# Kernel optimization log

Hardware: AMD Instinct MI355X
Metric: run time of the kernel (lower is better)

## Reference

```python
import jax, jax.numpy as jnp
import numpy as np

N, K, M = 4096, 128, 512  # conformers, dihedrals, atoms


def setup_inputs() -> dict:
    key = jax.random.key(0)
    k1, k2 = jax.random.split(key)
    inp = jax.random.normal(k1, (N, K), dtype=jnp.float32)          # target dihedral deltas (rad)
    pos0 = jax.random.normal(k2, (N, M, 3), dtype=jnp.float32)      # initial conformer coordinates
    base = jnp.arange(K, dtype=jnp.int32)
    # chain molecule: dihedral k defined by atoms (k, k+1, k+2, k+3)
    angles = jnp.stack([base, base + 1, base + 2, base + 3], axis=1)  # (K, 4)
    # rdkit toBeMovedIdxList on a chain for bond (k+1, k+2): atoms k+3 .. M-1 move
    move_mask = jnp.arange(M)[None, :] > (base + 2)[:, None]          # (K, M) bool
    return {"input": inp, "pos0": pos0, "angles": angles, "move_mask": move_mask}


def _rot_matrix(theta, axis):
    # rdkit Transform3D::SetRotation: R = (1-cos)*aa^T + [[c,-sZ,sY],[sZ,c,-sX],[-sY,sX,c]]
    cosT = jnp.cos(theta)
    sinT = jnp.sin(theta)
    t = 1.0 - cosT
    outer = t[:, None, None] * axis[:, :, None] * axis[:, None, :]   # (N,3,3)
    X, Y, Z = axis[:, 0], axis[:, 1], axis[:, 2]
    mat1 = jnp.stack(
        [cosT, -sinT * Z, sinT * Y,
         sinT * Z, cosT, -sinT * X,
         -sinT * Y, sinT * X, cosT], axis=1
    ).reshape(-1, 3, 3)
    return outer + mat1


def _step(pos, x):
    ang, mask, theta = x                       # (4,), (M,), (N,)
    p = jnp.take(pos, ang, axis=1)             # (N,4,3) gather of i,j,k,l atoms
    rIJ = p[:, 1] - p[:, 0]
    rJK = p[:, 2] - p[:, 1]
    rKL = p[:, 3] - p[:, 2]
    nIJK = jnp.cross(rIJ, rJK)
    nJKL = jnp.cross(rJK, rKL)
    m = jnp.cross(nIJK, rJK)
    nrm = lambda v: jnp.linalg.norm(v, axis=-1)
    sin_arg = jnp.sum(m * nJKL, axis=-1) / (nrm(nJKL) * nrm(m))
    cos_arg = jnp.sum(nIJK * nJKL, axis=-1) / (nrm(nIJK) * nrm(nJKL))
    values = theta + jnp.arctan2(sin_arg, cos_arg)   # rotation angle per conformer
    begin = p[:, 1]                                   # rotation axis origin (atom j)
    d = p[:, 2] - p[:, 1]
    # torch.nn.functional.normalize with eps=1e-12
    axis = d / jnp.maximum(jnp.linalg.norm(d, axis=-1, keepdims=True), 1e-12)
    R = _rot_matrix(values, axis)                     # (N,3,3)
    rotated = jnp.einsum('nij,nmj->nmi', R, pos - begin[:, None, :]) + begin[:, None, :]
    pos = jnp.where(mask[None, :, None], rotated, pos)
    return pos, None


def reference(input, pos0, angles, move_mask):
    xs = (angles, move_mask, input.T)                 # scan over K dihedrals (sequential recurrence)
    pos, _ = jax.lax.scan(_step, pos0, xs)
    return pos
```

## Files before the change

### kernel.cpp

```cpp
#include <hip/hip_runtime.h>


#define NK 128
#define NM 512
#define NMOL 4096
#define TPB 256
#define WPB 4
#define MPW 2

struct Aff { float qw, qx, qy, qz, tx, ty, tz; };

__device__ __forceinline__ void qrot(float qw, float qx, float qy, float qz,
                                     float vx, float vy, float vz,
                                     float& ox, float& oy, float& oz) {
    const float ux = qy*vz - qz*vy + qw*vx;
    const float uy = qz*vx - qx*vz + qw*vy;
    const float uz = qx*vy - qy*vx + qw*vz;
    ox = vx + 2.f*(qy*uz - qz*uy);
    oy = vy + 2.f*(qz*ux - qx*uz);
    oz = vz + 2.f*(qx*uy - qy*ux);
}

__device__ __forceinline__ Aff aff_compose(const Aff& Q, const Aff& P) {
    Aff r;
    r.qw = Q.qw*P.qw - Q.qx*P.qx - Q.qy*P.qy - Q.qz*P.qz;
    r.qx = Q.qw*P.qx + Q.qx*P.qw + Q.qy*P.qz - Q.qz*P.qy;
    r.qy = Q.qw*P.qy - Q.qx*P.qz + Q.qy*P.qw + Q.qz*P.qx;
    r.qz = Q.qw*P.qz + Q.qx*P.qy - Q.qy*P.qx + Q.qz*P.qw;
    float rx, ry, rz;
    qrot(Q.qw, Q.qx, Q.qy, Q.qz, P.tx, P.ty, P.tz, rx, ry, rz);
    r.tx = rx + Q.tx; r.ty = ry + Q.ty; r.tz = rz + Q.tz;
    return r;
}

#define SHFL_AFF_UP32(D, S, off)                                         \
    D.qw = __shfl_up(S.qw, off, 32); D.qx = __shfl_up(S.qx, off, 32);    \
    D.qy = __shfl_up(S.qy, off, 32); D.qz = __shfl_up(S.qz, off, 32);    \
    D.tx = __shfl_up(S.tx, off, 32); D.ty = __shfl_up(S.ty, off, 32);    \
    D.tz = __shfl_up(S.tz, off, 32);

#define BUILD_STEP(j, OUT) do {                                               \
    const float cxx = ny[(j)+1]*nz[(j)] - nz[(j)+1]*ny[(j)];                  \
    const float cxy = nz[(j)+1]*nx[(j)] - nx[(j)+1]*nz[(j)];                  \
    const float cxz = nx[(j)+1]*ny[(j)] - ny[(j)+1]*nx[(j)];                  \
    const float g   = cxx*vx[(j)+1] + cxy*vy[(j)+1] + cxz*vz[(j)+1];          \
    const float dnn = nx[(j)]*nx[(j)+1] + ny[(j)]*ny[(j)+1] + nz[(j)]*nz[(j)+1]; \
    const float r12 = rsqrtf(fmaxf(Ln[(j)]*Ln[(j)+1], 1e-30f));               \
    const float ira = rsqrtf(fmaxf(Lv[(j)+1], 1e-24f));                       \
    const float cphi = dnn*r12, sphi = g*r12*ira;                             \
    const float sth = __sinf(th[(j)]), cth = __cosf(th[(j)]);                 \
    const float c = cth*cphi - sth*sphi, s = sth*cphi + cth*sphi;             \
    const float hc = sqrtf(fmaxf(0.f, 0.5f*(1.f + c)));                       \
    const float hs = copysignf(sqrtf(fmaxf(0.f, 0.5f*(1.f - c))), s);         \
    const float hsa = hs*ira;                                                 \
    OUT.qw = hc; OUT.qx = vx[(j)+1]*hsa; OUT.qy = vy[(j)+1]*hsa; OUT.qz = vz[(j)+1]*hsa; \
    float rx, ry, rz;                                                         \
    qrot(OUT.qw, OUT.qx, OUT.qy, OUT.qz, A[3*(j)+3], A[3*(j)+4], A[3*(j)+5], rx, ry, rz); \
    OUT.tx = A[3*(j)+3]-rx; OUT.ty = A[3*(j)+4]-ry; OUT.tz = A[3*(j)+5]-rz;   \
} while (0)

__global__ __launch_bounds__(TPB, 2) void dihedral_seg2_kernel(
    const float* __restrict__ theta,
    const float* __restrict__ pos0,
    float* __restrict__ out)
{
    const int tid  = threadIdx.x;
    const int lane = tid & 63;
    const int wid  = tid >> 6;
    const int seg  = lane >> 5;
    const int sl   = lane & 31;
    const int mol  = blockIdx.x * (WPB * MPW) + wid * MPW + seg;

    const float4* __restrict__ pb4 = (const float4*)(pos0 + (size_t)mol * (NM*3));
    float4*       __restrict__ ob4 = (float4*)(out  + (size_t)mol * (NM*3));

    __shared__ float sA[WPB][MPW][400];
    __shared__ float sO[WPB][MPW][400];

    const bool ex = (sl < 3);
    float4 h0 = pb4[sl], h1 = pb4[sl + 32], h2 = pb4[sl + 64];
    float4 h3; if (ex) h3 = pb4[96 + sl];
    const float4 th4 = ((const float4*)(theta + (size_t)mol * NK))[sl];
    float4 T0a, T0b, T0c, T1a, T1b, T1c, T2a, T2b, T2c;
    { const int b = 99 + 3*sl;        T0a = pb4[b]; T0b = pb4[b+1]; T0c = pb4[b+2]; }
    { const int b = 99 + 3*(sl + 32); T1a = pb4[b]; T1b = pb4[b+1]; T1c = pb4[b+2]; }
    const bool has3 = (sl < 31);
    if (has3) { const int b = 99 + 3*(sl + 64); T2a = pb4[b]; T2b = pb4[b+1]; T2c = pb4[b+2]; }

    float4* sA4 = (float4*)sA[wid][seg];
    sA4[sl] = h0; sA4[sl + 32] = h1; sA4[sl + 64] = h2;
    if (ex) sA4[96 + sl] = h3;

    float A[21];
    {
        const float2* ap2 = (const float2*)&sA[wid][seg][sl * 12];
        #pragma unroll
        for (int i = 0; i < 10; ++i) { const float2 v = ap2[i]; A[2*i] = v.x; A[2*i+1] = v.y; }
        A[20] = sA[wid][seg][sl * 12 + 20];
    }

    float vx[6], vy[6], vz[6];
    #pragma unroll
    for (int i = 0; i < 6; ++i) {
        vx[i] = A[3*i+3] - A[3*i];
        vy[i] = A[3*i+4] - A[3*i+1];
        vz[i] = A[3*i+5] - A[3*i+2];
    }
    float nx[5], ny[5], nz[5], Ln[5];
    #pragma unroll
    for (int i = 0; i < 5; ++i) {
        nx[i] = vy[i]*vz[i+1] - vz[i]*vy[i+1];
        ny[i] = vz[i]*vx[i+1] - vx[i]*vz[i+1];
        nz[i] = vx[i]*vy[i+1] - vy[i]*vx[i+1];
        Ln[i] = nx[i]*nx[i] + ny[i]*ny[i] + nz[i]*nz[i];
    }
    float Lv[5];
    #pragma unroll
    for (int i = 1; i < 5; ++i) Lv[i] = vx[i]*vx[i] + vy[i]*vy[i] + vz[i]*vz[i];
    const float th[4] = {th4.x, th4.y, th4.z, th4.w};

    Aff B0;   BUILD_STEP(0, B0);
    Aff Bt;   BUILD_STEP(1, Bt);
    Aff C01  = aff_compose(B0, Bt);
    BUILD_STEP(2, Bt);
    Aff C012 = aff_compose(C01, Bt);
    BUILD_STEP(3, Bt);
    Aff S    = aff_compose(C012, Bt);

    #pragma unroll
    for (int off = 1; off < 32; off <<= 1) {
        Aff Q; SHFL_AFF_UP32(Q, S, off);
        if (sl >= off) S = aff_compose(Q, S);
    }
    Aff E; SHFL_AFF_UP32(E, S, 1);
    if (sl == 0) { E.qw = 1.f; E.qx = E.qy = E.qz = 0.f; E.tx = E.ty = E.tz = 0.f; }
    const Aff P0 = aff_compose(E, B0);
    const Aff P1 = aff_compose(E, C01);
    const Aff P2 = aff_compose(E, C012);

    {
        float ox, oy, oz;
        float* op = &sO[wid][seg][12*sl + 9];
        qrot(P0.qw, P0.qx, P0.qy, P0.qz, A[9],  A[10], A[11], ox, oy, oz);
        op[0] = ox + P0.tx; op[1] = oy + P0.ty; op[2] = oz + P0.tz;
        qrot(P1.qw, P1.qx, P1.qy, P1.qz, A[12], A[13], A[14], ox, oy, oz);
        op[3] = ox + P1.tx; op[4] = oy + P1.ty; op[5] = oz + P1.tz;
        qrot(P2.qw, P2.qx, P2.qy, P2.qz, A[15], A[16], A[17], ox, oy, oz);
        op[6] = ox + P2.tx; op[7] = oy + P2.ty; op[8] = oz + P2.tz;
        qrot(S.qw, S.qx, S.qy, S.qz, A[18], A[19], A[20], ox, oy, oz);
        op[9] = ox + S.tx;  op[10] = oy + S.ty; op[11] = oz + S.tz;
    }
    if (sl < 9) sO[wid][seg][sl] = sA[wid][seg][sl];
    if (sl == 31) {
        float ox, oy, oz;
        qrot(S.qw, S.qx, S.qy, S.qz, sA[wid][seg][393], sA[wid][seg][394], sA[wid][seg][395], ox, oy, oz);
        sO[wid][seg][393] = ox + S.tx; sO[wid][seg][394] = oy + S.ty; sO[wid][seg][395] = oz + S.tz;
    }

    Aff F;
    F.qw = __shfl(S.qw, 31, 32); F.qx = __shfl(S.qx, 31, 32);
    F.qy = __shfl(S.qy, 31, 32); F.qz = __shfl(S.qz, 31, 32);
    F.tx = __shfl(S.tx, 31, 32); F.ty = __shfl(S.ty, 31, 32);
    F.tz = __shfl(S.tz, 31, 32);
    const float f00 = 1.f - 2.f*(F.qy*F.qy + F.qz*F.qz);
    const float f01 = 2.f*(F.qx*F.qy - F.qw*F.qz);
    const float f02 = 2.f*(F.qx*F.qz + F.qw*F.qy);
    const float f10 = 2.f*(F.qx*F.qy + F.qw*F.qz);
    const float f11 = 1.f - 2.f*(F.qx*F.qx + F.qz*F.qz);
    const float f12 = 2.f*(F.qy*F.qz - F.qw*F.qx);
    const float f20 = 2.f*(F.qx*F.qz - F.qw*F.qy);
    const float f21 = 2.f*(F.qy*F.qz + F.qw*F.qx);
    const float f22 = 1.f - 2.f*(F.qx*F.qx + F.qy*F.qy);

    const float4* sO4 = (const float4*)sO[wid][seg];
    ob4[sl] = sO4[sl]; ob4[sl + 32] = sO4[sl + 32]; ob4[sl + 64] = sO4[sl + 64];
    if (ex) ob4[96 + sl] = sO4[96 + sl];

    #define TAIL_EMIT(b, va, vb, vc)                                          \
    do {                                                                      \
        const float x0=va.x, y0=va.y, z0=va.z;                                \
        const float x1=va.w, y1=vb.x, z1=vb.y;                                \
        const float x2=vb.z, y2=vb.w, z2=vc.x;                                \
        const float x3=vc.y, y3=vc.z, z3=vc.w;                                \
        float4 o0, o1, o2;                                                    \
        o0.x = f00*x0+f01*y0+f02*z0+F.tx; o0.y = f10*x0+f11*y0+f12*z0+F.ty;   \
        o0.z = f20*x0+f21*y0+f22*z0+F.tz; o0.w = f00*x1+f01*y1+f02*z1+F.tx;   \
        o1.x = f10*x1+f11*y1+f12*z1+F.ty; o1.y = f20*x1+f21*y1+f22*z1+F.tz;   \
        o1.z = f00*x2+f01*y2+f02*z2+F.tx; o1.w = f10*x2+f11*y2+f12*z2+F.ty;   \
        o2.x = f20*x2+f21*y2+f22*z2+F.tz; o2.y = f00*x3+f01*y3+f02*z3+F.tx;   \
        o2.z = f10*x3+f11*y3+f12*z3+F.ty; o2.w = f20*x3+f21*y3+f22*z3+F.tz;   \
        ob4[(b)] = o0; ob4[(b)+1] = o1; ob4[(b)+2] = o2;                      \
    } while (0)

    TAIL_EMIT(99 + 3*sl,        T0a, T0b, T0c);
    TAIL_EMIT(99 + 3*(sl + 32), T1a, T1b, T1c);
    if (has3) TAIL_EMIT(99 + 3*(sl + 64), T2a, T2b, T2c);
    #undef TAIL_EMIT
}

extern "C" void kernel_launch(void* const* d_in, const int* in_sizes, int n_in,
                              void* d_out, int out_size, void* d_ws, size_t ws_size,
                              hipStream_t stream) {
    const float* theta = (const float*)d_in[0];
    const float* pos0  = (const float*)d_in[1];
    float* out = (float*)d_out;
    dihedral_seg2_kernel<<<NMOL / (WPB * MPW), TPB, 0, stream>>>(theta, pos0, out);
}
```

Measured before the change: 17.67 us.

## Process two molecules per half-wave sequentially with prefetch of the second

Each 32-lane segment now handles two molecules in turn instead of one. The head and theta loads for the second molecule are issued before the first is computed, and its tail loads are issued after the first phase. Block size halves to 128 threads while the grid size stays the same, so there are half as many warps in total, each doing double work. The goal is to overlap memory latency with compute inside a warp, at the cost of lower occupancy and higher register pressure.

```diff
diff --git a/kernel.cpp b/kernel.cpp
--- a/kernel.cpp
+++ b/kernel.cpp
@@ -4,9 +4,7 @@
 #define NK 128
 #define NM 512
 #define NMOL 4096
-#define TPB 256
-#define WPB 4
-#define MPW 2
+#define TPB 128
 
 struct Aff { float qw, qx, qy, qz, tx, ty, tz; };
 
@@ -59,7 +57,7 @@
     OUT.tx = A[3*(j)+3]-rx; OUT.ty = A[3*(j)+4]-ry; OUT.tz = A[3*(j)+5]-rz;   \
 } while (0)
 
-__global__ __launch_bounds__(TPB, 2) void dihedral_seg2_kernel(
+__global__ __launch_bounds__(TPB, 1) void dihedral_pipe_seg_kernel(
     const float* __restrict__ theta,
     const float* __restrict__ pos0,
     float* __restrict__ out)
@@ -69,133 +67,152 @@
     const int wid  = tid >> 6;
     const int seg  = lane >> 5;
     const int sl   = lane & 31;
-    const int mol  = blockIdx.x * (WPB * MPW) + wid * MPW + seg;
-
-    const float4* __restrict__ pb4 = (const float4*)(pos0 + (size_t)mol * (NM*3));
-    float4*       __restrict__ ob4 = (float4*)(out  + (size_t)mol * (NM*3));
-
-    __shared__ float sA[WPB][MPW][400];
-    __shared__ float sO[WPB][MPW][400];
-
-    const bool ex = (sl < 3);
-    float4 h0 = pb4[sl], h1 = pb4[sl + 32], h2 = pb4[sl + 64];
-    float4 h3; if (ex) h3 = pb4[96 + sl];
-    const float4 th4 = ((const float4*)(theta + (size_t)mol * NK))[sl];
-    float4 T0a, T0b, T0c, T1a, T1b, T1c, T2a, T2b, T2c;
-    { const int b = 99 + 3*sl;        T0a = pb4[b]; T0b = pb4[b+1]; T0c = pb4[b+2]; }
-    { const int b = 99 + 3*(sl + 32); T1a = pb4[b]; T1b = pb4[b+1]; T1c = pb4[b+2]; }
+    const int base = (blockIdx.x * 2 + wid) * 4 + seg * 2;
+    const int molA = base, molB = base + 1;
+
+    const float4* __restrict__ pbA = (const float4*)(pos0 + (size_t)molA * (NM*3));
+    float4*       __restrict__ obA = (float4*)(out  + (size_t)molA * (NM*3));
+    const float4* __restrict__ pbB = (const float4*)(pos0 + (size_t)molB * (NM*3));
+    float4*       __restrict__ obB = (float4*)(out  + (size_t)molB * (NM*3));
+
+    __shared__ float sAm[2][2][400];
+    __shared__ float sOm[2][2][400];
+    float* __restrict__ sa = sAm[wid][seg];
+    float* __restrict__ so = sOm[wid][seg];
+
+    const bool ex   = (sl < 3);
     const bool has3 = (sl < 31);
-    if (has3) { const int b = 99 + 3*(sl + 64); T2a = pb4[b]; T2b = pb4[b+1]; T2c = pb4[b+2]; }
-
-    float4* sA4 = (float4*)sA[wid][seg];
-    sA4[sl] = h0; sA4[sl + 32] = h1; sA4[sl + 64] = h2;
-    if (ex) sA4[96 + sl] = h3;
-
-    float A[21];
-    {
-        const float2* ap2 = (const float2*)&sA[wid][seg][sl * 12];
-        #pragma unroll
-        for (int i = 0; i < 10; ++i) { const float2 v = ap2[i]; A[2*i] = v.x; A[2*i+1] = v.y; }
-        A[20] = sA[wid][seg][sl * 12 + 20];
-    }
-
-    float vx[6], vy[6], vz[6];
-    #pragma unroll
-    for (int i = 0; i < 6; ++i) {
-        vx[i] = A[3*i+3] - A[3*i];
-        vy[i] = A[3*i+4] - A[3*i+1];
-        vz[i] = A[3*i+5] - A[3*i+2];
-    }
-    float nx[5], ny[5], nz[5], Ln[5];
-    #pragma unroll
-    for (int i = 0; i < 5; ++i) {
-        nx[i] = vy[i]*vz[i+1] - vz[i]*vy[i+1];
-        ny[i] = vz[i]*vx[i+1] - vx[i]*vz[i+1];
-        nz[i] = vx[i]*vy[i+1] - vy[i]*vx[i+1];
-        Ln[i] = nx[i]*nx[i] + ny[i]*ny[i] + nz[i]*nz[i];
-    }
-    float Lv[5];
-    #pragma unroll
-    for (int i = 1; i < 5; ++i) Lv[i] = vx[i]*vx[i] + vy[i]*vy[i] + vz[i]*vz[i];
-    const float th[4] = {th4.x, th4.y, th4.z, th4.w};
-
-    Aff B0;   BUILD_STEP(0, B0);
-    Aff Bt;   BUILD_STEP(1, Bt);
-    Aff C01  = aff_compose(B0, Bt);
-    BUILD_STEP(2, Bt);
-    Aff C012 = aff_compose(C01, Bt);
-    BUILD_STEP(3, Bt);
-    Aff S    = aff_compose(C012, Bt);
-
-    #pragma unroll
-    for (int off = 1; off < 32; off <<= 1) {
-        Aff Q; SHFL_AFF_UP32(Q, S, off);
-        if (sl >= off) S = aff_compose(Q, S);
-    }
-    Aff E; SHFL_AFF_UP32(E, S, 1);
-    if (sl == 0) { E.qw = 1.f; E.qx = E.qy = E.qz = 0.f; E.tx = E.ty = E.tz = 0.f; }
-    const Aff P0 = aff_compose(E, B0);
-    const Aff P1 = aff_compose(E, C01);
-    const Aff P2 = aff_compose(E, C012);
-
-    {
-        float ox, oy, oz;
-        float* op = &sO[wid][seg][12*sl + 9];
-        qrot(P0.qw, P0.qx, P0.qy, P0.qz, A[9],  A[10], A[11], ox, oy, oz);
-        op[0] = ox + P0.tx; op[1] = oy + P0.ty; op[2] = oz + P0.tz;
-        qrot(P1.qw, P1.qx, P1.qy, P1.qz, A[12], A[13], A[14], ox, oy, oz);
-        op[3] = ox + P1.tx; op[4] = oy + P1.ty; op[5] = oz + P1.tz;
-        qrot(P2.qw, P2.qx, P2.qy, P2.qz, A[15], A[16], A[17], ox, oy, oz);
-        op[6] = ox + P2.tx; op[7] = oy + P2.ty; op[8] = oz + P2.tz;
-        qrot(S.qw, S.qx, S.qy, S.qz, A[18], A[19], A[20], ox, oy, oz);
-        op[9] = ox + S.tx;  op[10] = oy + S.ty; op[11] = oz + S.tz;
-    }
-    if (sl < 9) sO[wid][seg][sl] = sA[wid][seg][sl];
-    if (sl == 31) {
-        float ox, oy, oz;
-        qrot(S.qw, S.qx, S.qy, S.qz, sA[wid][seg][393], sA[wid][seg][394], sA[wid][seg][395], ox, oy, oz);
-        sO[wid][seg][393] = ox + S.tx; sO[wid][seg][394] = oy + S.ty; sO[wid][seg][395] = oz + S.tz;
-    }
-
-    Aff F;
-    F.qw = __shfl(S.qw, 31, 32); F.qx = __shfl(S.qx, 31, 32);
-    F.qy = __shfl(S.qy, 31, 32); F.qz = __shfl(S.qz, 31, 32);
-    F.tx = __shfl(S.tx, 31, 32); F.ty = __shfl(S.ty, 31, 32);
-    F.tz = __shfl(S.tz, 31, 32);
-    const float f00 = 1.f - 2.f*(F.qy*F.qy + F.qz*F.qz);
-    const float f01 = 2.f*(F.qx*F.qy - F.qw*F.qz);
-    const float f02 = 2.f*(F.qx*F.qz + F.qw*F.qy);
-    const float f10 = 2.f*(F.qx*F.qy + F.qw*F.qz);
-    const float f11 = 1.f - 2.f*(F.qx*F.qx + F.qz*F.qz);
-    const float f12 = 2.f*(F.qy*F.qz - F.qw*F.qx);
-    const float f20 = 2.f*(F.qx*F.qz - F.qw*F.qy);
-    const float f21 = 2.f*(F.qy*F.qz + F.qw*F.qx);
-    const float f22 = 1.f - 2.f*(F.qx*F.qx + F.qy*F.qy);
-
-    const float4* sO4 = (const float4*)sO[wid][seg];
-    ob4[sl] = sO4[sl]; ob4[sl + 32] = sO4[sl + 32]; ob4[sl + 64] = sO4[sl + 64];
-    if (ex) ob4[96 + sl] = sO4[96 + sl];
-
-    #define TAIL_EMIT(b, va, vb, vc)                                          \
-    do {                                                                      \
-        const float x0=va.x, y0=va.y, z0=va.z;                                \
-        const float x1=va.w, y1=vb.x, z1=vb.y;                                \
-        const float x2=vb.z, y2=vb.w, z2=vc.x;                                \
-        const float x3=vc.y, y3=vc.z, z3=vc.w;                                \
-        float4 o0, o1, o2;                                                    \
-        o0.x = f00*x0+f01*y0+f02*z0+F.tx; o0.y = f10*x0+f11*y0+f12*z0+F.ty;   \
-        o0.z = f20*x0+f21*y0+f22*z0+F.tz; o0.w = f00*x1+f01*y1+f02*z1+F.tx;   \
-        o1.x = f10*x1+f11*y1+f12*z1+F.ty; o1.y = f20*x1+f21*y1+f22*z1+F.tz;   \
-        o1.z = f00*x2+f01*y2+f02*z2+F.tx; o1.w = f10*x2+f11*y2+f12*z2+F.ty;   \
-        o2.x = f20*x2+f21*y2+f22*z2+F.tz; o2.y = f00*x3+f01*y3+f02*z3+F.tx;   \
-        o2.z = f10*x3+f11*y3+f12*z3+F.ty; o2.w = f20*x3+f21*y3+f22*z3+F.tz;   \
-        ob4[(b)] = o0; ob4[(b)+1] = o1; ob4[(b)+2] = o2;                      \
-    } while (0)
-
-    TAIL_EMIT(99 + 3*sl,        T0a, T0b, T0c);
-    TAIL_EMIT(99 + 3*(sl + 32), T1a, T1b, T1c);
-    if (has3) TAIL_EMIT(99 + 3*(sl + 64), T2a, T2b, T2c);
-    #undef TAIL_EMIT
+
+    auto PHASE = [&](float4 h0, float4 h1, float4 h2, float4 h3,
+                     const float4 th4, const float4* T, float4* __restrict__ ob4) {
+        float4* sa4 = (float4*)sa;
+        sa4[sl] = h0; sa4[sl + 32] = h1; sa4[sl + 64] = h2;
+        if (ex) sa4[96 + sl] = h3;
+
+        float A[21];
+        {
+            const float2* ap2 = (const float2*)&sa[sl * 12];
+            #pragma unroll
+            for (int i = 0; i < 10; ++i) { const float2 v = ap2[i]; A[2*i] = v.x; A[2*i+1] = v.y; }
+            A[20] = sa[sl * 12 + 20];
+        }
+        float vx[6], vy[6], vz[6];
+        #pragma unroll
+        for (int i = 0; i < 6; ++i) {
+            vx[i] = A[3*i+3] - A[3*i];
+            vy[i] = A[3*i+4] - A[3*i+1];
+            vz[i] = A[3*i+5] - A[3*i+2];
+        }
+        float nx[5], ny[5], nz[5], Ln[5];
+        #pragma unroll
+        for (int i = 0; i < 5; ++i) {
+            nx[i] = vy[i]*vz[i+1] - vz[i]*vy[i+1];
+            ny[i] = vz[i]*vx[i+1] - vx[i]*vz[i+1];
+            nz[i] = vx[i]*vy[i+1] - vy[i]*vx[i+1];
+            Ln[i] = nx[i]*nx[i] + ny[i]*ny[i] + nz[i]*nz[i];
+        }
+        float Lv[5];
+        #pragma unroll
+        for (int i = 1; i < 5; ++i) Lv[i] = vx[i]*vx[i] + vy[i]*vy[i] + vz[i]*vz[i];
+        const float th[4] = {th4.x, th4.y, th4.z, th4.w};
+
+        Aff B0;   BUILD_STEP(0, B0);
+        Aff Bt;   BUILD_STEP(1, Bt);
+        Aff C01  = aff_compose(B0, Bt);
+        BUILD_STEP(2, Bt);
+        Aff C012 = aff_compose(C01, Bt);
+        BUILD_STEP(3, Bt);
+        Aff S    = aff_compose(C012, Bt);
+
+        #pragma unroll
+        for (int off = 1; off < 32; off <<= 1) {
+            Aff Q; SHFL_AFF_UP32(Q, S, off);
+            if (sl >= off) S = aff_compose(Q, S);
+        }
+        Aff E; SHFL_AFF_UP32(E, S, 1);
+        if (sl == 0) { E.qw = 1.f; E.qx = E.qy = E.qz = 0.f; E.tx = E.ty = E.tz = 0.f; }
+        const Aff P0 = aff_compose(E, B0);
+        const Aff P1 = aff_compose(E, C01);
+        const Aff P2 = aff_compose(E, C012);
+
+        {
+            float ox, oy, oz;
+            float* op = &so[12*sl + 9];
+            qrot(P0.qw, P0.qx, P0.qy, P0.qz, A[9],  A[10], A[11], ox, oy, oz);
+            op[0] = ox + P0.tx; op[1] = oy + P0.ty; op[2] = oz + P0.tz;
+            qrot(P1.qw, P1.qx, P1.qy, P1.qz, A[12], A[13], A[14], ox, oy, oz);
+            op[3] = ox + P1.tx; op[4] = oy + P1.ty; op[5] = oz + P1.tz;
+            qrot(P2.qw, P2.qx, P2.qy, P2.qz, A[15], A[16], A[17], ox, oy, oz);
+            op[6] = ox + P2.tx; op[7] = oy + P2.ty; op[8] = oz + P2.tz;
+            qrot(S.qw, S.qx, S.qy, S.qz, A[18], A[19], A[20], ox, oy, oz);
+            op[9] = ox + S.tx;  op[10] = oy + S.ty; op[11] = oz + S.tz;
+        }
+        if (sl < 9) so[sl] = sa[sl];
+        if (sl == 31) {
+            float ox, oy, oz;
+            qrot(S.qw, S.qx, S.qy, S.qz, sa[393], sa[394], sa[395], ox, oy, oz);
+            so[393] = ox + S.tx; so[394] = oy + S.ty; so[395] = oz + S.tz;
+        }
+
+        Aff F;
+        F.qw = __shfl(S.qw, 31, 32); F.qx = __shfl(S.qx, 31, 32);
+        F.qy = __shfl(S.qy, 31, 32); F.qz = __shfl(S.qz, 31, 32);
+        F.tx = __shfl(S.tx, 31, 32); F.ty = __shfl(S.ty, 31, 32);
+        F.tz = __shfl(S.tz, 31, 32);
+        const float f00 = 1.f - 2.f*(F.qy*F.qy + F.qz*F.qz);
+        const float f01 = 2.f*(F.qx*F.qy - F.qw*F.qz);
+        const float f02 = 2.f*(F.qx*F.qz + F.qw*F.qy);
+        const float f10 = 2.f*(F.qx*F.qy + F.qw*F.qz);
+        const float f11 = 1.f - 2.f*(F.qx*F.qx + F.qz*F.qz);
+        const float f12 = 2.f*(F.qy*F.qz - F.qw*F.qx);
+        const float f20 = 2.f*(F.qx*F.qz - F.qw*F.qy);
+        const float f21 = 2.f*(F.qy*F.qz + F.qw*F.qx);
+        const float f22 = 1.f - 2.f*(F.qx*F.qx + F.qy*F.qy);
+
+        const float4* so4 = (const float4*)so;
+        ob4[sl] = so4[sl]; ob4[sl + 32] = so4[sl + 32]; ob4[sl + 64] = so4[sl + 64];
+        if (ex) ob4[96 + sl] = so4[96 + sl];
+
+        #define TAIL_EMIT(b, va, vb, vc)                                      \
+        do {                                                                  \
+            const float x0=va.x, y0=va.y, z0=va.z;                            \
+            const float x1=va.w, y1=vb.x, z1=vb.y;                            \
+            const float x2=vb.z, y2=vb.w, z2=vc.x;                            \
+            const float x3=vc.y, y3=vc.z, z3=vc.w;                            \
+            float4 o0, o1, o2;                                                \
+            o0.x = f00*x0+f01*y0+f02*z0+F.tx; o0.y = f10*x0+f11*y0+f12*z0+F.ty; \
+            o0.z = f20*x0+f21*y0+f22*z0+F.tz; o0.w = f00*x1+f01*y1+f02*z1+F.tx; \
+            o1.x = f10*x1+f11*y1+f12*z1+F.ty; o1.y = f20*x1+f21*y1+f22*z1+F.tz; \
+            o1.z = f00*x2+f01*y2+f02*z2+F.tx; o1.w = f10*x2+f11*y2+f12*z2+F.ty; \
+            o2.x = f20*x2+f21*y2+f22*z2+F.tz; o2.y = f00*x3+f01*y3+f02*z3+F.tx; \
+            o2.z = f10*x3+f11*y3+f12*z3+F.ty; o2.w = f20*x3+f21*y3+f22*z3+F.tz; \
+            ob4[(b)] = o0; ob4[(b)+1] = o1; ob4[(b)+2] = o2;                  \
+        } while (0)
+        TAIL_EMIT(99 + 3*sl,        T[0], T[1], T[2]);
+        TAIL_EMIT(99 + 3*(sl + 32), T[3], T[4], T[5]);
+        if (has3) TAIL_EMIT(99 + 3*(sl + 64), T[6], T[7], T[8]);
+        #undef TAIL_EMIT
+    };
+
+    float4 hA0 = pbA[sl], hA1 = pbA[sl + 32], hA2 = pbA[sl + 64];
+    float4 hA3; if (ex) hA3 = pbA[96 + sl];
+    const float4 thA4 = ((const float4*)(theta + (size_t)molA * NK))[sl];
+    float4 TA[9];
+    { const int b = 99 + 3*sl;        TA[0] = pbA[b]; TA[1] = pbA[b+1]; TA[2] = pbA[b+2]; }
+    { const int b = 99 + 3*(sl + 32); TA[3] = pbA[b]; TA[4] = pbA[b+1]; TA[5] = pbA[b+2]; }
+    if (has3) { const int b = 99 + 3*(sl + 64); TA[6] = pbA[b]; TA[7] = pbA[b+1]; TA[8] = pbA[b+2]; }
+    float4 hB0 = pbB[sl], hB1 = pbB[sl + 32], hB2 = pbB[sl + 64];
+    float4 hB3; if (ex) hB3 = pbB[96 + sl];
+    const float4 thB4 = ((const float4*)(theta + (size_t)molB * NK))[sl];
+
+    PHASE(hA0, hA1, hA2, hA3, thA4, TA, obA);
+
+    float4 TB[9];
+    { const int b = 99 + 3*sl;        TB[0] = pbB[b]; TB[1] = pbB[b+1]; TB[2] = pbB[b+2]; }
+    { const int b = 99 + 3*(sl + 32); TB[3] = pbB[b]; TB[4] = pbB[b+1]; TB[5] = pbB[b+2]; }
+    if (has3) { const int b = 99 + 3*(sl + 64); TB[6] = pbB[b]; TB[7] = pbB[b+1]; TB[8] = pbB[b+2]; }
+
+    PHASE(hB0, hB1, hB2, hB3, thB4, TB, obB);
 }
 
 extern "C" void kernel_launch(void* const* d_in, const int* in_sizes, int n_in,
@@ -204,5 +221,5 @@
     const float* theta = (const float*)d_in[0];
     const float* pos0  = (const float*)d_in[1];
     float* out = (float*)d_out;
-    dihedral_seg2_kernel<<<NMOL / (WPB * MPW), TPB, 0, stream>>>(theta, pos0, out);
-}
+    dihedral_pipe_seg_kernel<<<NMOL / 8, TPB, 0, stream>>>(theta, pos0, out);
+}
```

Result: slower. 20.92 us (+18.4%).

## Replace affine-transform scan with quaternion scan plus bond-vector prefix sums

Applied to the files above, without the earlier changes.

Changes the parallel prefix from 7-component rigid transforms (quaternion plus translation) to pure 4-component quaternion products. Positions are rebuilt by rotating bond vectors and prefix-summing them, with separate even and odd chains for atoms k+3 and k+4. This cuts shuffle traffic and compose arithmetic in the scan but adds a second 6-float shuffle scan. Accumulating translations by summation may change rounding slightly.

```diff
diff --git a/kernel.cpp b/kernel.cpp
--- a/kernel.cpp
+++ b/kernel.cpp
@@ -8,38 +8,32 @@
 #define WPB 4
 #define MPW 2
 
-struct Aff { float qw, qx, qy, qz, tx, ty, tz; };
-
-__device__ __forceinline__ void qrot(float qw, float qx, float qy, float qz,
-                                     float vx, float vy, float vz,
-                                     float& ox, float& oy, float& oz) {
-    const float ux = qy*vz - qz*vy + qw*vx;
-    const float uy = qz*vx - qx*vz + qw*vy;
-    const float uz = qx*vy - qy*vx + qw*vz;
-    ox = vx + 2.f*(qy*uz - qz*uy);
-    oy = vy + 2.f*(qz*ux - qx*uz);
-    oz = vz + 2.f*(qx*uy - qy*ux);
-}
-
-__device__ __forceinline__ Aff aff_compose(const Aff& Q, const Aff& P) {
-    Aff r;
-    r.qw = Q.qw*P.qw - Q.qx*P.qx - Q.qy*P.qy - Q.qz*P.qz;
-    r.qx = Q.qw*P.qx + Q.qx*P.qw + Q.qy*P.qz - Q.qz*P.qy;
-    r.qy = Q.qw*P.qy - Q.qx*P.qz + Q.qy*P.qw + Q.qz*P.qx;
-    r.qz = Q.qw*P.qz + Q.qx*P.qy - Q.qy*P.qx + Q.qz*P.qw;
-    float rx, ry, rz;
-    qrot(Q.qw, Q.qx, Q.qy, Q.qz, P.tx, P.ty, P.tz, rx, ry, rz);
-    r.tx = rx + Q.tx; r.ty = ry + Q.ty; r.tz = rz + Q.tz;
+struct Q4 { float w, x, y, z; };
+
+__device__ __forceinline__ Q4 qmul(const Q4& a, const Q4& b) {
+    Q4 r;
+    r.w = a.w*b.w - a.x*b.x - a.y*b.y - a.z*b.z;
+    r.x = a.w*b.x + a.x*b.w + a.y*b.z - a.z*b.y;
+    r.y = a.w*b.y - a.x*b.z + a.y*b.w + a.z*b.x;
+    r.z = a.w*b.z + a.x*b.y - a.y*b.x + a.z*b.w;
     return r;
 }
 
-#define SHFL_AFF_UP32(D, S, off)                                         \
-    D.qw = __shfl_up(S.qw, off, 32); D.qx = __shfl_up(S.qx, off, 32);    \
-    D.qy = __shfl_up(S.qy, off, 32); D.qz = __shfl_up(S.qz, off, 32);    \
-    D.tx = __shfl_up(S.tx, off, 32); D.ty = __shfl_up(S.ty, off, 32);    \
-    D.tz = __shfl_up(S.tz, off, 32);
-
-#define BUILD_STEP(j, OUT) do {                                               \
+__device__ __forceinline__ void qrotv(const Q4& q, float vx, float vy, float vz,
+                                      float& ox, float& oy, float& oz) {
+    const float ux = q.y*vz - q.z*vy + q.w*vx;
+    const float uy = q.z*vx - q.x*vz + q.w*vy;
+    const float uz = q.x*vy - q.y*vx + q.w*vz;
+    ox = vx + 2.f*(q.y*uz - q.z*uy);
+    oy = vy + 2.f*(q.z*ux - q.x*uz);
+    oz = vz + 2.f*(q.x*uy - q.y*ux);
+}
+
+#define SHFL_Q_UP32(D, S, off)                                           \
+    D.w = __shfl_up(S.w, off, 32); D.x = __shfl_up(S.x, off, 32);        \
+    D.y = __shfl_up(S.y, off, 32); D.z = __shfl_up(S.z, off, 32);
+
+#define BUILD_Q(j, OUT) do {                                                  \
     const float cxx = ny[(j)+1]*nz[(j)] - nz[(j)+1]*ny[(j)];                  \
     const float cxy = nz[(j)+1]*nx[(j)] - nx[(j)+1]*nz[(j)];                  \
     const float cxz = nx[(j)+1]*ny[(j)] - ny[(j)+1]*nx[(j)];                  \
@@ -53,13 +47,10 @@
     const float hc = sqrtf(fmaxf(0.f, 0.5f*(1.f + c)));                       \
     const float hs = copysignf(sqrtf(fmaxf(0.f, 0.5f*(1.f - c))), s);         \
     const float hsa = hs*ira;                                                 \
-    OUT.qw = hc; OUT.qx = vx[(j)+1]*hsa; OUT.qy = vy[(j)+1]*hsa; OUT.qz = vz[(j)+1]*hsa; \
-    float rx, ry, rz;                                                         \
-    qrot(OUT.qw, OUT.qx, OUT.qy, OUT.qz, A[3*(j)+3], A[3*(j)+4], A[3*(j)+5], rx, ry, rz); \
-    OUT.tx = A[3*(j)+3]-rx; OUT.ty = A[3*(j)+4]-ry; OUT.tz = A[3*(j)+5]-rz;   \
+    OUT.w = hc; OUT.x = vx[(j)+1]*hsa; OUT.y = vy[(j)+1]*hsa; OUT.z = vz[(j)+1]*hsa; \
 } while (0)
 
-__global__ __launch_bounds__(TPB, 2) void dihedral_seg2_kernel(
+__global__ __launch_bounds__(TPB, 2) void dihedral_qscan_kernel(
     const float* __restrict__ theta,
     const float* __restrict__ pos0,
     float* __restrict__ out)
@@ -74,8 +65,10 @@
     const float4* __restrict__ pb4 = (const float4*)(pos0 + (size_t)mol * (NM*3));
     float4*       __restrict__ ob4 = (float4*)(out  + (size_t)mol * (NM*3));
 
-    __shared__ float sA[WPB][MPW][400];
-    __shared__ float sO[WPB][MPW][400];
+    __shared__ float sAm[WPB][MPW][400];
+    __shared__ float sOm[WPB][MPW][400];
+    float* __restrict__ sa   = sAm[wid][seg];
+    float* __restrict__ sout = sOm[wid][seg];
 
     const bool ex = (sl < 3);
     float4 h0 = pb4[sl], h1 = pb4[sl + 32], h2 = pb4[sl + 64];
@@ -87,16 +80,16 @@
     const bool has3 = (sl < 31);
     if (has3) { const int b = 99 + 3*(sl + 64); T2a = pb4[b]; T2b = pb4[b+1]; T2c = pb4[b+2]; }
 
-    float4* sA4 = (float4*)sA[wid][seg];
-    sA4[sl] = h0; sA4[sl + 32] = h1; sA4[sl + 64] = h2;
-    if (ex) sA4[96 + sl] = h3;
+    float4* sa4 = (float4*)sa;
+    sa4[sl] = h0; sa4[sl + 32] = h1; sa4[sl + 64] = h2;
+    if (ex) sa4[96 + sl] = h3;
 
     float A[21];
     {
-        const float2* ap2 = (const float2*)&sA[wid][seg][sl * 12];
+        const float2* ap2 = (const float2*)&sa[sl * 12];
         #pragma unroll
         for (int i = 0; i < 10; ++i) { const float2 v = ap2[i]; A[2*i] = v.x; A[2*i+1] = v.y; }
-        A[20] = sA[wid][seg][sl * 12 + 20];
+        A[20] = sa[sl * 12 + 20];
     }
 
     float vx[6], vy[6], vz[6];
@@ -119,62 +112,80 @@
     for (int i = 1; i < 5; ++i) Lv[i] = vx[i]*vx[i] + vy[i]*vy[i] + vz[i]*vz[i];
     const float th[4] = {th4.x, th4.y, th4.z, th4.w};
 
-    Aff B0;   BUILD_STEP(0, B0);
-    Aff Bt;   BUILD_STEP(1, Bt);
-    Aff C01  = aff_compose(B0, Bt);
-    BUILD_STEP(2, Bt);
-    Aff C012 = aff_compose(C01, Bt);
-    BUILD_STEP(3, Bt);
-    Aff S    = aff_compose(C012, Bt);
+    Q4 q0, q1, q2, q3;
+    BUILD_Q(0, q0); BUILD_Q(1, q1); BUILD_Q(2, q2); BUILD_Q(3, q3);
+    const Q4 Q01   = qmul(q0, q1);
+    const Q4 Q012  = qmul(Q01, q2);
+    Q4 S           = qmul(Q012, q3);
 
     #pragma unroll
     for (int off = 1; off < 32; off <<= 1) {
-        Aff Q; SHFL_AFF_UP32(Q, S, off);
-        if (sl >= off) S = aff_compose(Q, S);
-    }
-    Aff E; SHFL_AFF_UP32(E, S, 1);
-    if (sl == 0) { E.qw = 1.f; E.qx = E.qy = E.qz = 0.f; E.tx = E.ty = E.tz = 0.f; }
-    const Aff P0 = aff_compose(E, B0);
-    const Aff P1 = aff_compose(E, C01);
-    const Aff P2 = aff_compose(E, C012);
+        Q4 Qp; SHFL_Q_UP32(Qp, S, off);
+        if (sl >= off) S = qmul(Qp, S);
+    }
+    Q4 E; SHFL_Q_UP32(E, S, 1);
+    if (sl == 0) { E.w = 1.f; E.x = E.y = E.z = 0.f; }
+
+    const Q4 Pq0 = qmul(E, q0);
+    const Q4 Pq1 = qmul(E, Q01);
+    const Q4 Pq2 = qmul(E, Q012);
+
+    float d0x,d0y,d0z, d1x,d1y,d1z, d2x,d2y,d2z, d3x,d3y,d3z;
+    qrotv(Pq0, A[9]-A[3],   A[10]-A[4],  A[11]-A[5],  d0x,d0y,d0z);
+    qrotv(Pq1, A[12]-A[6],  A[13]-A[7],  A[14]-A[8],  d1x,d1y,d1z);
+    qrotv(Pq2, A[15]-A[9],  A[16]-A[10], A[17]-A[11], d2x,d2y,d2z);
+    qrotv(S,   A[18]-A[12], A[19]-A[13], A[20]-A[14], d3x,d3y,d3z);
+
+    float sex = d0x + d2x, sey = d0y + d2y, sez = d0z + d2z;
+    float sox = d1x + d3x, soy = d1y + d3y, soz = d1z + d3z;
+    #pragma unroll
+    for (int off = 1; off < 32; off <<= 1) {
+        const float ax = __shfl_up(sex, off, 32), ay = __shfl_up(sey, off, 32), az = __shfl_up(sez, off, 32);
+        const float bx = __shfl_up(sox, off, 32), by = __shfl_up(soy, off, 32), bz = __shfl_up(soz, off, 32);
+        if (sl >= off) { sex += ax; sey += ay; sez += az; sox += bx; soy += by; soz += bz; }
+    }
+
+    const float p1x = sa[3], p1y = sa[4], p1z = sa[5];
+    const float p2x = sa[6], p2y = sa[7], p2z = sa[8];
+    const float f3x = p1x + sex - d2x, f3y = p1y + sey - d2y, f3z = p1z + sez - d2z;
+    const float f5x = p1x + sex,       f5y = p1y + sey,       f5z = p1z + sez;
+    const float f4x = p2x + sox - d3x, f4y = p2y + soy - d3y, f4z = p2z + soz - d3z;
+    const float f6x = p2x + sox,       f6y = p2y + soy,       f6z = p2z + soz;
 
     {
-        float ox, oy, oz;
-        float* op = &sO[wid][seg][12*sl + 9];
-        qrot(P0.qw, P0.qx, P0.qy, P0.qz, A[9],  A[10], A[11], ox, oy, oz);
-        op[0] = ox + P0.tx; op[1] = oy + P0.ty; op[2] = oz + P0.tz;
-        qrot(P1.qw, P1.qx, P1.qy, P1.qz, A[12], A[13], A[14], ox, oy, oz);
-        op[3] = ox + P1.tx; op[4] = oy + P1.ty; op[5] = oz + P1.tz;
-        qrot(P2.qw, P2.qx, P2.qy, P2.qz, A[15], A[16], A[17], ox, oy, oz);
-        op[6] = ox + P2.tx; op[7] = oy + P2.ty; op[8] = oz + P2.tz;
-        qrot(S.qw, S.qx, S.qy, S.qz, A[18], A[19], A[20], ox, oy, oz);
-        op[9] = ox + S.tx;  op[10] = oy + S.ty; op[11] = oz + S.tz;
-    }
-    if (sl < 9) sO[wid][seg][sl] = sA[wid][seg][sl];
+        float* op = &sout[12*sl + 9];
+        op[0] = f3x; op[1]  = f3y; op[2]  = f3z;
+        op[3] = f4x; op[4]  = f4y; op[5]  = f4z;
+        op[6] = f5x; op[7]  = f5y; op[8]  = f5z;
+        op[9] = f6x; op[10] = f6y; op[11] = f6z;
+    }
+    if (sl < 9) sout[sl] = sa[sl];
+
+    float tFx = 0.f, tFy = 0.f, tFz = 0.f;
     if (sl == 31) {
-        float ox, oy, oz;
-        qrot(S.qw, S.qx, S.qy, S.qz, sA[wid][seg][393], sA[wid][seg][394], sA[wid][seg][395], ox, oy, oz);
-        sO[wid][seg][393] = ox + S.tx; sO[wid][seg][394] = oy + S.ty; sO[wid][seg][395] = oz + S.tz;
-    }
-
-    Aff F;
-    F.qw = __shfl(S.qw, 31, 32); F.qx = __shfl(S.qx, 31, 32);
-    F.qy = __shfl(S.qy, 31, 32); F.qz = __shfl(S.qz, 31, 32);
-    F.tx = __shfl(S.tx, 31, 32); F.ty = __shfl(S.ty, 31, 32);
-    F.tz = __shfl(S.tz, 31, 32);
-    const float f00 = 1.f - 2.f*(F.qy*F.qy + F.qz*F.qz);
-    const float f01 = 2.f*(F.qx*F.qy - F.qw*F.qz);
-    const float f02 = 2.f*(F.qx*F.qz + F.qw*F.qy);
-    const float f10 = 2.f*(F.qx*F.qy + F.qw*F.qz);
-    const float f11 = 1.f - 2.f*(F.qx*F.qx + F.qz*F.qz);
-    const float f12 = 2.f*(F.qy*F.qz - F.qw*F.qx);
-    const float f20 = 2.f*(F.qx*F.qz - F.qw*F.qy);
-    const float f21 = 2.f*(F.qy*F.qz + F.qw*F.qx);
-    const float f22 = 1.f - 2.f*(F.qx*F.qx + F.qy*F.qy);
-
-    const float4* sO4 = (const float4*)sO[wid][seg];
-    ob4[sl] = sO4[sl]; ob4[sl + 32] = sO4[sl + 32]; ob4[sl + 64] = sO4[sl + 64];
-    if (ex) ob4[96 + sl] = sO4[96 + sl];
+        float rx, ry, rz;
+        qrotv(S, sa[384], sa[385], sa[386], rx, ry, rz);
+        tFx = f4x - rx; tFy = f4y - ry; tFz = f4z - rz;
+        qrotv(S, sa[393], sa[394], sa[395], rx, ry, rz);
+        sout[393] = rx + tFx; sout[394] = ry + tFy; sout[395] = rz + tFz;
+    }
+    Q4 Fq;
+    Fq.w = __shfl(S.w, 31, 32); Fq.x = __shfl(S.x, 31, 32);
+    Fq.y = __shfl(S.y, 31, 32); Fq.z = __shfl(S.z, 31, 32);
+    const float Ftx = __shfl(tFx, 31, 32), Fty = __shfl(tFy, 31, 32), Ftz = __shfl(tFz, 31, 32);
+    const float f00 = 1.f - 2.f*(Fq.y*Fq.y + Fq.z*Fq.z);
+    const float f01 = 2.f*(Fq.x*Fq.y - Fq.w*Fq.z);
+    const float f02 = 2.f*(Fq.x*Fq.z + Fq.w*Fq.y);
+    const float f10 = 2.f*(Fq.x*Fq.y + Fq.w*Fq.z);
+    const float f11 = 1.f - 2.f*(Fq.x*Fq.x + Fq.z*Fq.z);
+    const float f12 = 2.f*(Fq.y*Fq.z - Fq.w*Fq.x);
+    const float f20 = 2.f*(Fq.x*Fq.z - Fq.w*Fq.y);
+    const float f21 = 2.f*(Fq.y*Fq.z + Fq.w*Fq.x);
+    const float f22 = 1.f - 2.f*(Fq.x*Fq.x + Fq.y*Fq.y);
+
+    const float4* so4 = (const float4*)sout;
+    ob4[sl] = so4[sl]; ob4[sl + 32] = so4[sl + 32]; ob4[sl + 64] = so4[sl + 64];
+    if (ex) ob4[96 + sl] = so4[96 + sl];
 
     #define TAIL_EMIT(b, va, vb, vc)                                          \
     do {                                                                      \
@@ -183,12 +194,12 @@
         const float x2=vb.z, y2=vb.w, z2=vc.x;                                \
         const float x3=vc.y, y3=vc.z, z3=vc.w;                                \
         float4 o0, o1, o2;                                                    \
-        o0.x = f00*x0+f01*y0+f02*z0+F.tx; o0.y = f10*x0+f11*y0+f12*z0+F.ty;   \
-        o0.z = f20*x0+f21*y0+f22*z0+F.tz; o0.w = f00*x1+f01*y1+f02*z1+F.tx;   \
-        o1.x = f10*x1+f11*y1+f12*z1+F.ty; o1.y = f20*x1+f21*y1+f22*z1+F.tz;   \
-        o1.z = f00*x2+f01*y2+f02*z2+F.tx; o1.w = f10*x2+f11*y2+f12*z2+F.ty;   \
-        o2.x = f20*x2+f21*y2+f22*z2+F.tz; o2.y = f00*x3+f01*y3+f02*z3+F.tx;   \
-        o2.z = f10*x3+f11*y3+f12*z3+F.ty; o2.w = f20*x3+f21*y3+f22*z3+F.tz;   \
+        o0.x = f00*x0+f01*y0+f02*z0+Ftx; o0.y = f10*x0+f11*y0+f12*z0+Fty;     \
+        o0.z = f20*x0+f21*y0+f22*z0+Ftz; o0.w = f00*x1+f01*y1+f02*z1+Ftx;     \
+        o1.x = f10*x1+f11*y1+f12*z1+Fty; o1.y = f20*x1+f21*y1+f22*z1+Ftz;     \
+        o1.z = f00*x2+f01*y2+f02*z2+Ftx; o1.w = f10*x2+f11*y2+f12*z2+Fty;     \
+        o2.x = f20*x2+f21*y2+f22*z2+Ftz; o2.y = f00*x3+f01*y3+f02*z3+Ftx;     \
+        o2.z = f10*x3+f11*y3+f12*z3+Fty; o2.w = f20*x3+f21*y3+f22*z3+Ftz;     \
         ob4[(b)] = o0; ob4[(b)+1] = o1; ob4[(b)+2] = o2;                      \
     } while (0)
 
@@ -204,5 +215,5 @@
     const float* theta = (const float*)d_in[0];
     const float* pos0  = (const float*)d_in[1];
     float* out = (float*)d_out;
-    dihedral_seg2_kernel<<<NMOL / (WPB * MPW), TPB, 0, stream>>>(theta, pos0, out);
-}
+    dihedral_qscan_kernel<<<NMOL / (WPB * MPW), TPB, 0, stream>>>(theta, pos0, out);
+}
```

After: 17.20 us. -2.7%, faster.
